# Optimization experiments

Measured on AMD Instinct MI355X. Metric: run time of the kernel, lower is better.

## Reference

```python
import jax, jax.numpy as jnp
import numpy as np

N_GRAPHS = 2048
BN_EPS = 1e-5


def _lin_init(k, fan_in, fan_out):
    kw, kb = jax.random.split(k)
    s = 1.0 / np.sqrt(fan_in)
    w = jax.random.uniform(kw, (fan_in, fan_out), minval=-s, maxval=s, dtype=jnp.float32)
    b = jax.random.uniform(kb, (fan_out,), minval=-s, maxval=s, dtype=jnp.float32)
    return w, b


def setup_inputs() -> dict:
    key = jax.random.key(0)
    ks = jax.random.split(key, 16)
    N, E, F, H, C = 100000, 600000, 7, 128, 2
    inp = {}
    inp["x"] = jax.random.normal(ks[0], (N, F), dtype=jnp.float32)
    inp["edge_index"] = jax.random.randint(ks[1], (2, E), 0, N)
    inp["edge_attr"] = jax.random.normal(ks[2], (E,), dtype=jnp.float32)  # ignored by GINConv
    inp["batch"] = jnp.sort(jax.random.randint(ks[3], (N,), 0, N_GRAPHS))
    # GINConv inner MLPs: [in, H, H]
    inp["g1_w1"], inp["g1_b1"] = _lin_init(ks[4], F, H)
    inp["g1_w2"], inp["g1_b2"] = _lin_init(ks[5], H, H)
    inp["g2_w1"], inp["g2_b1"] = _lin_init(ks[6], H, H)
    inp["g2_w2"], inp["g2_b2"] = _lin_init(ks[7], H, H)
    inp["g3_w1"], inp["g3_b1"] = _lin_init(ks[8], H, H)
    inp["g3_w2"], inp["g3_b2"] = _lin_init(ks[9], H, H)
    # JumpingKnowledge('cat') projection: 3H -> H
    inp["jk_w"], inp["jk_b"] = _lin_init(ks[10], 3 * H, H)
    # classifier MLP [H, H, C] with batch_norm on hidden layer
    inp["c1_w"], inp["c1_b"] = _lin_init(ks[11], H, H)
    inp["bn_g"] = jnp.ones((H,), jnp.float32)
    inp["bn_b"] = jnp.zeros((H,), jnp.float32)
    inp["c2_w"], inp["c2_b"] = _lin_init(ks[12], H, C)
    return inp


def reference(x, edge_index, edge_attr, batch,
              g1_w1, g1_b1, g1_w2, g1_b2,
              g2_w1, g2_b1, g2_w2, g2_b2,
              g3_w1, g3_b1, g3_w2, g3_b2,
              jk_w, jk_b, c1_w, c1_b, bn_g, bn_b, c2_w, c2_b):
    src, dst = edge_index[0], edge_index[1]
    N = x.shape[0]

    def gin_conv(h, w1, b1, w2, b2):
        # sum aggregation of neighbor messages; eps=0 -> (1+eps)*x + aggr = x + aggr
        agg = jax.ops.segment_sum(h[src], dst, num_segments=N)
        z = h + agg
        return jax.nn.relu(z @ w1 + b1) @ w2 + b2  # inner MLP, plain last layer

    # BasicGNN applies act (ReLU) after each conv; dropout=eval (identity)
    h1 = jax.nn.relu(gin_conv(x, g1_w1, g1_b1, g1_w2, g1_b2))
    h2 = jax.nn.relu(gin_conv(h1, g2_w1, g2_b1, g2_w2, g2_b2))
    h3 = jax.nn.relu(gin_conv(h2, g3_w1, g3_b1, g3_w2, g3_b2))

    h = jnp.concatenate([h1, h2, h3], axis=-1) @ jk_w + jk_b  # jk='cat' + final lin
    g = jax.ops.segment_sum(h, batch, num_segments=N_GRAPHS)  # global_add_pool -> [G, H]

    z = g @ c1_w + c1_b
    mu = z.mean(axis=0)
    var = z.var(axis=0)
    z = (z - mu) * jax.lax.rsqrt(var + BN_EPS) * bn_g + bn_b  # batch_norm (batch stats)
    z = jax.nn.relu(z)
    return z @ c2_w + c2_b  # [G, num_classes]
```

## Files before the change

kernel.cpp:

```cpp
#include <hip/hip_runtime.h>

#define NGRAPH 2048
#define EIDX_CAP 1024

typedef __attribute__((ext_vector_type(4))) float f32x4;
typedef __attribute__((ext_vector_type(8))) _Float16 h16x8;
typedef __attribute__((ext_vector_type(2))) _Float16 h16x2;

__global__ __launch_bounds__(256) void scan_onepass(
    const int* __restrict__ deg, int* __restrict__ rowstart, int* __restrict__ cursor,
    unsigned* __restrict__ scanst, int N, int E, int nchunk)
{
  __shared__ int tmp[256];
  __shared__ int sh_chunk;
  __shared__ int sh_exc;
  int tid = threadIdx.x;
  if (tid == 0) sh_chunk = (int)atomicAdd(&scanst[nchunk], 1u);
  __syncthreads();
  int cb = sh_chunk;
  int i = cb * 256 + tid;
  int v = (i < N) ? deg[i] : 0;
  tmp[tid] = v;
  __syncthreads();
#pragma unroll
  for (int off = 1; off < 256; off <<= 1) {
    int t = (tid >= off) ? tmp[tid - off] : 0;
    __syncthreads();
    tmp[tid] += t;
    __syncthreads();
  }
  int aggregate = tmp[255];

  if (tid == 0) {
    const unsigned VMASK = (1u << 30) - 1u;
    if (cb == 0) {
      atomicExch(&scanst[0], (2u << 30) | (unsigned)aggregate);
      sh_exc = 0;
    } else {
      atomicExch(&scanst[cb], (1u << 30) | (unsigned)aggregate);
      int excv = 0;
      int j = cb - 1;
      while (j >= 0) {
        unsigned s;
        do { s = atomicAdd(&scanst[j], 0u); } while ((s >> 30) == 0u);
        excv += (int)(s & VMASK);
        if ((s >> 30) == 2u) break;
        --j;
      }
      sh_exc = excv;
      atomicExch(&scanst[cb], (2u << 30) | (unsigned)(excv + aggregate));
    }
  }
  __syncthreads();
  int exc = sh_exc;
  if (i < N) {
    int rs = exc + tmp[tid] - v;
    rowstart[i] = rs;
    cursor[i] = rs;
  }
  if (cb == nchunk - 1 && tid == 0) rowstart[N] = E;
}

__global__ __launch_bounds__(256) void fill_eidx(
    const int* __restrict__ src, const int* __restrict__ dst,
    int* __restrict__ cursor, int* __restrict__ eidx, int E)
{
  int e = blockIdx.x * 256 + threadIdx.x;
  if (e >= E) return;
  int d = dst[e];
  int pos = atomicAdd(&cursor[d], 1);
  eidx[pos] = src[e];
}

struct WPs {
  const float* w[5];
  _Float16* hi[5];
  _Float16* lo[5];
};
__global__ __launch_bounds__(256) void prep_hist(
    WPs p, const float* __restrict__ x, _Float16* __restrict__ x8h, int N,
    const int* __restrict__ dst, int* __restrict__ deg, int E,
    const int* __restrict__ batch, int* __restrict__ gstart,
    float* __restrict__ bnstat)
{
  int g = blockIdx.x * 256 + threadIdx.x;
  if (g < E) {
    atomicAdd(&deg[dst[g]], 1);
    return;
  }
  int q = g - E;
  if (q < 5 * 16384) {
    int m = q >> 14;
    int j = q & 16383;
    int c = j >> 3, e = j & 7;
    int t = c >> 8, kc = (c >> 6) & 3, lane = c & 63;
    int n = t * 16 + (lane & 15);
    int k = kc * 32 + (lane >> 4) * 8 + e;
    float w = p.w[m][k * 128 + n];
    _Float16 h = (_Float16)w;
    p.hi[m][j] = h;
    p.lo[m][j] = (_Float16)(w - (float)h);
    return;
  }
  q -= 5 * 16384;
  if (q < N * 8) {
    int v = q >> 3, j = q & 7;
    x8h[q] = (_Float16)((j < 7) ? x[(long)v * 7 + j] : 0.f);
    return;
  }
  q -= N * 8;
  if (q < 256) { bnstat[q] = 0.f; return; }
  q -= 256;
  if (q < N) {
    int b = batch[q];
    int bp = (q > 0) ? batch[q - 1] : -1;
    for (int gg = bp + 1; gg <= b; ++gg) gstart[gg] = q;
    if (q == N - 1)
      for (int gg = b + 1; gg <= NGRAPH; ++gg) gstart[gg] = N;
  }
}

__device__ inline void mfma_pass(
    const _Float16* __restrict__ zbuf,
    const _Float16* __restrict__ Whi, const _Float16* __restrict__ Wlo,
    int rw, int m16, int quad, int lane, f32x4 acc[8])
{
  int r = rw + m16;
  const _Float16* zrow = &zbuf[r * 128];
#pragma unroll
  for (int kc = 0; kc < 4; ++kc) {
    int cidx = kc * 4 + quad;
    h16x8 ah = *(const h16x8*)&zrow[((cidx + r) & 15) * 8];
#pragma unroll
    for (int t = 0; t < 8; ++t) {
      long cb = ((t * 4 + kc) * 64 + lane) * 8;
      h16x8 bh = *(const h16x8*)&Whi[cb];
      h16x8 bl = *(const h16x8*)&Wlo[cb];
      acc[t] = __builtin_amdgcn_mfma_f32_16x16x32_f16(ah, bh, acc[t], 0, 0, 0);
      acc[t] = __builtin_amdgcn_mfma_f32_16x16x32_f16(ah, bl, acc[t], 0, 0, 0);
    }
  }
}

__global__ __launch_bounds__(256, 5) void fused_gin(
    const _Float16* __restrict__ H, const int* __restrict__ rowstart,
    const int* __restrict__ eidx,
    const _Float16* __restrict__ W1hi, const _Float16* __restrict__ W1lo,
    const float* __restrict__ B1,
    const _Float16* __restrict__ W2hi, const _Float16* __restrict__ W2lo,
    const float* __restrict__ B2,
    _Float16* __restrict__ Out, int M)
{
  __shared__ _Float16 zbuf[64 * 128];
  __shared__ int sh_rs[65];
  __shared__ int sh_ei[EIDX_CAP];
  int tid = threadIdx.x;
  int rbase = blockIdx.x * 64;

  if (tid < 65) {
    int v = rbase + tid;
    sh_rs[tid] = rowstart[(v < M) ? v : M];
  }
  __syncthreads();
  int e_begin = sh_rs[0];
  int cnt = sh_rs[64] - e_begin;
  if (cnt <= EIDX_CAP) {
    for (int i = tid; i < cnt; i += 256) sh_ei[i] = eidx[e_begin + i];
  }
  __syncthreads();

  {
    int sub = tid & 15;
    int ng = tid >> 4;
    const _Float16* Hc = H + sub * 8;
    if (cnt <= EIDX_CAP) {
#pragma unroll 1
      for (int it = 0; it < 4; ++it) {
        int r = it * 16 + ng;
        int v = rbase + r;
        int vc = (v < M) ? v : (M - 1);
        h16x8 sv = *(const h16x8*)&Hc[(long)vc * 128];
        float a0[8], a1[8];
#pragma unroll
        for (int j = 0; j < 8; ++j) { a0[j] = (float)sv[j]; a1[j] = 0.f; }
        int e = sh_rs[r] - e_begin;
        int e1 = sh_rs[r + 1] - e_begin;
#pragma unroll 1
        for (; e < e1; e += 8) {
          int last = e1 - 1;
          int s0 = sh_ei[e];
          int s1 = sh_ei[(e + 1 < e1) ? e + 1 : last];
          int s2 = sh_ei[(e + 2 < e1) ? e + 2 : last];
          int s3 = sh_ei[(e + 3 < e1) ? e + 3 : last];
          int s4 = sh_ei[(e + 4 < e1) ? e + 4 : last];
          int s5 = sh_ei[(e + 5 < e1) ? e + 5 : last];
          int s6 = sh_ei[(e + 6 < e1) ? e + 6 : last];
          int s7 = sh_ei[(e + 7 < e1) ? e + 7 : last];
          float m1 = (e + 1 < e1) ? 1.f : 0.f;
          float m2 = (e + 2 < e1) ? 1.f : 0.f;
          float m3 = (e + 3 < e1) ? 1.f : 0.f;
          float m4 = (e + 4 < e1) ? 1.f : 0.f;
          float m5 = (e + 5 < e1) ? 1.f : 0.f;
          float m6 = (e + 6 < e1) ? 1.f : 0.f;
          float m7 = (e + 7 < e1) ? 1.f : 0.f;
          h16x8 h0 = *(const h16x8*)&Hc[(long)s0 * 128];
          h16x8 h1 = *(const h16x8*)&Hc[(long)s1 * 128];
          h16x8 h2 = *(const h16x8*)&Hc[(long)s2 * 128];
          h16x8 h3 = *(const h16x8*)&Hc[(long)s3 * 128];
          h16x8 h4 = *(const h16x8*)&Hc[(long)s4 * 128];
          h16x8 h5 = *(const h16x8*)&Hc[(long)s5 * 128];
          h16x8 h6 = *(const h16x8*)&Hc[(long)s6 * 128];
          h16x8 h7 = *(const h16x8*)&Hc[(long)s7 * 128];
#pragma unroll
          for (int j = 0; j < 8; ++j) {
            a0[j] += (float)h0[j] + m2 * (float)h2[j] + m4 * (float)h4[j] + m6 * (float)h6[j];
            a1[j] += m1 * (float)h1[j] + m3 * (float)h3[j] + m5 * (float)h5[j] + m7 * (float)h7[j];
          }
        }
        h16x8 zo;
#pragma unroll
        for (int j = 0; j < 8; ++j) zo[j] = (_Float16)(a0[j] + a1[j]);
        *(h16x8*)&zbuf[r * 128 + ((sub + r) & 15) * 8] = zo;
      }
    } else {
#pragma unroll 1
      for (int it = 0; it < 4; ++it) {
        int r = it * 16 + ng;
        int v = rbase + r;
        int vc = (v < M) ? v : (M - 1);
        h16x8 sv = *(const h16x8*)&Hc[(long)vc * 128];
        float a0[8], a1[8];
#pragma unroll
        for (int j = 0; j < 8; ++j) { a0[j] = (float)sv[j]; a1[j] = 0.f; }
        int e = sh_rs[r], e1 = sh_rs[r + 1];
        for (; e + 2 <= e1; e += 2) {
          int s0 = eidx[e], s1 = eidx[e + 1];
          h16x8 h0 = *(const h16x8*)&Hc[(long)s0 * 128];
          h16x8 h1 = *(const h16x8*)&Hc[(long)s1 * 128];
#pragma unroll
          for (int j = 0; j < 8; ++j) { a0[j] += (float)h0[j]; a1[j] += (float)h1[j]; }
        }
        if (e < e1) {
          int s = eidx[e];
          h16x8 h = *(const h16x8*)&Hc[(long)s * 128];
#pragma unroll
          for (int j = 0; j < 8; ++j) a1[j] += (float)h[j];
        }
        h16x8 zo;
#pragma unroll
        for (int j = 0; j < 8; ++j) zo[j] = (_Float16)(a0[j] + a1[j]);
        *(h16x8*)&zbuf[r * 128 + ((sub + r) & 15) * 8] = zo;
      }
    }
  }
  __syncthreads();

  int lane = tid & 63;
  int wv = tid >> 6;
  int m16 = lane & 15;
  int quad = lane >> 4;
  int rw = wv * 16;

  f32x4 acc[8];
#pragma unroll
  for (int t = 0; t < 8; ++t) acc[t] = (f32x4){0.f, 0.f, 0.f, 0.f};
  mfma_pass(zbuf, W1hi, W1lo, rw, m16, quad, lane, acc);

  float bias[8];
#pragma unroll
  for (int t = 0; t < 8; ++t) bias[t] = B1[t * 16 + m16];

#pragma unroll
  for (int i = 0; i < 4; ++i) {
    int r = rw + quad * 4 + i;
#pragma unroll
    for (int t = 0; t < 8; ++t) {
      int col = t * 16 + m16;
      int cidx = col >> 3;
      zbuf[r * 128 + ((cidx + r) & 15) * 8 + (col & 7)] =
          (_Float16)fmaxf(acc[t][i] + bias[t], 0.f);
    }
  }

#pragma unroll
  for (int t = 0; t < 8; ++t) acc[t] = (f32x4){0.f, 0.f, 0.f, 0.f};
  mfma_pass(zbuf, W2hi, W2lo, rw, m16, quad, lane, acc);

#pragma unroll
  for (int t = 0; t < 8; ++t) bias[t] = B2[t * 16 + m16];

#pragma unroll
  for (int i = 0; i < 4; ++i) {
    int r = rw + quad * 4 + i;
#pragma unroll
    for (int t = 0; t < 8; ++t) {
      int col = t * 16 + m16;
      int cidx = col >> 3;
      zbuf[r * 128 + ((cidx + r) & 15) * 8 + (col & 7)] =
          (_Float16)fmaxf(acc[t][i] + bias[t], 0.f);
    }
  }
  {
    int rr2 = tid >> 2, c4 = tid & 3;
    int r = rbase + rr2;
    if (r < M) {
#pragma unroll
      for (int it = 0; it < 4; ++it) {
        int cidx = it * 4 + c4;
        h16x8 vv = *(const h16x8*)&zbuf[rr2 * 128 + ((cidx + rr2) & 15) * 8];
        *(h16x8*)&Out[(long)r * 128 + cidx * 8] = vv;
      }
    }
  }
}

__global__ __launch_bounds__(256, 8) void fused_l1(
    const _Float16* __restrict__ x8h, const int* __restrict__ rowstart,
    const int* __restrict__ eidx,
    const float* __restrict__ W1, const float* __restrict__ B1,
    const _Float16* __restrict__ W2hi, const _Float16* __restrict__ W2lo,
    const float* __restrict__ B2, _Float16* __restrict__ Out, int M)
{
  __shared__ _Float16 ybuf[64 * 128];
  __shared__ float z1s[64][8];
  int tid = threadIdx.x;
  int rbase = blockIdx.x * 64;

  {
    int node = tid >> 2, sub = tid & 3;
    int v = rbase + node;
    int vc = (v < M) ? v : (M - 1);
    float a[8];
    if (sub == 0) {
      h16x8 sv = *(const h16x8*)&x8h[(long)vc * 8];
#pragma unroll
      for (int j = 0; j < 8; ++j) a[j] = (float)sv[j];
    } else {
#pragma unroll
      for (int j = 0; j < 8; ++j) a[j] = 0.f;
    }
    int e0 = rowstart[vc], e1 = rowstart[vc + 1];
    int e = e0 + sub;
    for (; e + 4 < e1; e += 8) {
      int s0 = eidx[e], s1 = eidx[e + 4];
      h16x8 h0 = *(const h16x8*)&x8h[(long)s0 * 8];
      h16x8 h1 = *(const h16x8*)&x8h[(long)s1 * 8];
#pragma unroll
      for (int j = 0; j < 8; ++j) a[j] += (float)h0[j] + (float)h1[j];
    }
    if (e < e1) {
      int s = eidx[e];
      h16x8 h = *(const h16x8*)&x8h[(long)s * 8];
#pragma unroll
      for (int j = 0; j < 8; ++j) a[j] += (float)h[j];
    }
#pragma unroll
    for (int j = 0; j < 8; ++j) {
      a[j] += __shfl_xor(a[j], 1, 64);
      a[j] += __shfl_xor(a[j], 2, 64);
    }
    if (sub == 0) {
#pragma unroll
      for (int j = 0; j < 8; ++j) z1s[node][j] = a[j];
    }
  }
  __syncthreads();

  {
    int c = tid & 127;
    int cidx = c >> 3, celt = c & 7;
    int rh0 = (tid >> 7) * 32;
    float w1r[7];
#pragma unroll
    for (int k = 0; k < 7; ++k) w1r[k] = W1[k * 128 + c];
    float b1 = B1[c];
#pragma unroll 4
    for (int rr = 0; rr < 32; ++rr) {
      int r = rh0 + rr;
      const float* zp = z1s[r];
      float a = b1;
#pragma unroll
      for (int k = 0; k < 7; ++k) a += zp[k] * w1r[k];
      ybuf[r * 128 + ((cidx + r) & 15) * 8 + celt] = (_Float16)fmaxf(a, 0.f);
    }
  }
  __syncthreads();

  int lane = tid & 63;
  int wv = tid >> 6;
  int m16 = lane & 15;
  int quad = lane >> 4;
  int rw = wv * 16;

  f32x4 acc[8];
#pragma unroll
  for (int t = 0; t < 8; ++t) acc[t] = (f32x4){0.f, 0.f, 0.f, 0.f};
  mfma_pass(ybuf, W2hi, W2lo, rw, m16, quad, lane, acc);

  float bias[8];
#pragma unroll
  for (int t = 0; t < 8; ++t) bias[t] = B2[t * 16 + m16];

#pragma unroll
  for (int i = 0; i < 4; ++i) {
    int r = rw + quad * 4 + i;
#pragma unroll
    for (int t = 0; t < 8; ++t) {
      int col = t * 16 + m16;
      int cidx = col >> 3;
      ybuf[r * 128 + ((cidx + r) & 15) * 8 + (col & 7)] =
          (_Float16)fmaxf(acc[t][i] + bias[t], 0.f);
    }
  }
  {
    int rr2 = tid >> 2, c4 = tid & 3;
    int r = rbase + rr2;
    if (r < M) {
#pragma unroll
      for (int it = 0; it < 4; ++it) {
        int cidx = it * 4 + c4;
        h16x8 vv = *(const h16x8*)&ybuf[rr2 * 128 + ((cidx + rr2) & 15) * 8];
        *(h16x8*)&Out[(long)r * 128 + cidx * 8] = vv;
      }
    }
  }
}

__global__ __launch_bounds__(256) void pool_direct(
    const _Float16* __restrict__ H1, const _Float16* __restrict__ H2,
    const _Float16* __restrict__ H3, const int* __restrict__ gstart,
    float* __restrict__ P)
{
  __shared__ float red[3 * 16 * 8 * 4];
  int g = blockIdx.x;
  int s = gstart[g], e = gstart[g + 1];
  int tid = threadIdx.x;
  int wv = tid >> 6, lane = tid & 63;
  int tbl = lane >> 4;
  int ch = lane & 15;
  float a[8];
#pragma unroll
  for (int j = 0; j < 8; ++j) a[j] = 0.f;
  if (tbl < 3) {
    const _Float16* A = (tbl == 0) ? H1 : ((tbl == 1) ? H2 : H3);
    const _Float16* Ac = A + ch * 8;
    for (int r = s + wv; r < e; r += 4) {
      h16x8 v = *(const h16x8*)&Ac[(long)r * 128];
#pragma unroll
      for (int j = 0; j < 8; ++j) a[j] += (float)v[j];
    }
#pragma unroll
    for (int j = 0; j < 8; ++j) red[((tbl * 16 + ch) * 8 + j) * 4 + wv] = a[j];
  }
  __syncthreads();
  for (int t = tid; t < 384; t += 256) {
    float4 rv = *(const float4*)&red[t * 4];
    P[(long)g * 384 + t] = rv.x + rv.y + rv.z + rv.w;
  }
}

__global__ __launch_bounds__(256) void jk_gemm(
    const float* __restrict__ P, const int* __restrict__ gstart,
    const float* __restrict__ W, const float* __restrict__ B,
    float* __restrict__ G)
{
  __shared__ float pl[768];
  int tid = threadIdx.x, blk = blockIdx.x;
  for (int o = tid; o < 768; o += 256) pl[o] = P[(long)blk * 768 + o];
  __syncthreads();
  int rr = tid >> 7;
  int col = tid & 127;
  int row = blk * 2 + rr;
  float cntv = (float)(gstart[row + 1] - gstart[row]);
  float acc = cntv * B[col];
#pragma unroll 8
  for (int k = 0; k < 384; ++k)
    acc += pl[rr * 384 + k] * W[k * 128 + col];
  G[(long)row * 128 + col] = acc;
}

__global__ __launch_bounds__(256) void gemm_bn(
    const float* __restrict__ Z,
    const float* __restrict__ W, const float* __restrict__ B,
    float* __restrict__ Out, float* __restrict__ bnstat, int M)
{
  __shared__ float wlds[128 * 128];
  int tid = threadIdx.x;
  {
    const float4* Ws = (const float4*)W;
    float4* Wd = (float4*)wlds;
#pragma unroll
    for (int i = 0; i < 16; ++i) Wd[i * 256 + tid] = Ws[i * 256 + tid];
  }
  __syncthreads();

  int rg = tid >> 5;
  int c0 = (tid & 31) * 4;
  int rbase = blockIdx.x * 64 + rg * 8;

  float acc[8][4];
#pragma unroll
  for (int i = 0; i < 8; ++i)
#pragma unroll
    for (int j = 0; j < 4; ++j) acc[i][j] = 0.f;

#pragma unroll 2
  for (int kc = 0; kc < 128; kc += 4) {
    float zv[8][4];
#pragma unroll
    for (int i = 0; i < 8; ++i) {
      float4 z = *(const float4*)&Z[(long)(rbase + i) * 128 + kc];
      zv[i][0] = z.x; zv[i][1] = z.y; zv[i][2] = z.z; zv[i][3] = z.w;
    }
#pragma unroll
    for (int kk = 0; kk < 4; ++kk) {
      float4 w = *(const float4*)&wlds[(kc + kk) * 128 + c0];
#pragma unroll
      for (int i = 0; i < 8; ++i) {
        float z = zv[i][kk];
        acc[i][0] += z * w.x; acc[i][1] += z * w.y;
        acc[i][2] += z * w.z; acc[i][3] += z * w.w;
      }
    }
  }

  float4 b = *(const float4*)&B[c0];
  float s[4] = {0.f, 0.f, 0.f, 0.f};
  float s2[4] = {0.f, 0.f, 0.f, 0.f};
#pragma unroll
  for (int i = 0; i < 8; ++i) {
    float4 o;
    o.x = acc[i][0] + b.x; o.y = acc[i][1] + b.y;
    o.z = acc[i][2] + b.z; o.w = acc[i][3] + b.w;
    *(float4*)&Out[(long)(rbase + i) * 128 + c0] = o;
    s[0] += o.x; s[1] += o.y; s[2] += o.z; s[3] += o.w;
    s2[0] += o.x * o.x; s2[1] += o.y * o.y; s2[2] += o.z * o.z; s2[3] += o.w * o.w;
  }
#pragma unroll
  for (int j = 0; j < 4; ++j) {
    atomicAdd(&bnstat[c0 + j], s[j]);
    atomicAdd(&bnstat[128 + c0 + j], s2[j]);
  }
}

__global__ __launch_bounds__(256) void bn_final(
    const float* __restrict__ ZC, const float* __restrict__ bnstat,
    const float* __restrict__ gma, const float* __restrict__ bta,
    const float* __restrict__ W2, const float* __restrict__ B2, float* __restrict__ out)
{
  __shared__ float scl[128], shf[128];
  int tid = threadIdx.x;
  if (tid < 128) {
    float mu = bnstat[tid] * (1.f / NGRAPH);
    float var = bnstat[128 + tid] * (1.f / NGRAPH) - mu * mu;
    float rs = rsqrtf(var + 1e-5f);
    float sc = gma[tid] * rs;
    scl[tid] = sc;
    shf[tid] = bta[tid] - mu * sc;
  }
  __syncthreads();
  int g = blockIdx.x * 256 + tid;
  if (g >= NGRAPH) return;
  float a0 = B2[0], a1 = B2[1];
#pragma unroll 4
  for (int h = 0; h < 128; ++h) {
    float zn = ZC[(long)g * 128 + h] * scl[h] + shf[h];
    zn = fmaxf(zn, 0.f);
    a0 += zn * W2[2 * h];
    a1 += zn * W2[2 * h + 1];
  }
  out[2 * g] = a0;
  out[2 * g + 1] = a1;
}

extern "C" void kernel_launch(void* const* d_in, const int* in_sizes, int n_in,
                              void* d_out, int out_size, void* d_ws, size_t ws_size,
                              hipStream_t stream)
{
  const float* x    = (const float*)d_in[0];
  const int*   ei   = (const int*)d_in[1];
  const int*   batch = (const int*)d_in[3];
  const float* g1w1 = (const float*)d_in[4];  const float* g1b1 = (const float*)d_in[5];
  const float* g1w2 = (const float*)d_in[6];  const float* g1b2 = (const float*)d_in[7];
  const float* g2w1 = (const float*)d_in[8];  const float* g2b1 = (const float*)d_in[9];
  const float* g2w2 = (const float*)d_in[10]; const float* g2b2 = (const float*)d_in[11];
  const float* g3w1 = (const float*)d_in[12]; const float* g3b1 = (const float*)d_in[13];
  const float* g3w2 = (const float*)d_in[14]; const float* g3b2 = (const float*)d_in[15];
  const float* jkw  = (const float*)d_in[16]; const float* jkb  = (const float*)d_in[17];
  const float* c1w  = (const float*)d_in[18]; const float* c1b  = (const float*)d_in[19];
  const float* bng  = (const float*)d_in[20]; const float* bnb  = (const float*)d_in[21];
  const float* c2w  = (const float*)d_in[22]; const float* c2b  = (const float*)d_in[23];

  const int N = in_sizes[3];
  const int E = in_sizes[1] / 2;
  const int* src = ei;
  const int* dst = ei + E;

  char* w = (char*)d_ws;
  auto alloc = [&](size_t bytes) {
    char* p = w;
    w += (bytes + 255) & ~(size_t)255;
    return p;
  };
  _Float16* hA = (_Float16*)alloc((size_t)N * 128 * 2);
  _Float16* hB = (_Float16*)alloc((size_t)N * 128 * 2);
  _Float16* hC = (_Float16*)alloc((size_t)N * 128 * 2);
  _Float16* x8h = (_Float16*)alloc((size_t)N * 8 * 2);
  float* P       = (float*)alloc((size_t)NGRAPH * 384 * 4);
  float* bnstat  = (float*)alloc(256 * 4);
  float* gbuf = (float*)alloc((size_t)NGRAPH * 128 * 4);
  float* zc   = (float*)alloc((size_t)NGRAPH * 128 * 4);
  int* deg      = (int*)alloc((size_t)N * 4);
  unsigned* scanst = (unsigned*)alloc((size_t)1024 * 4);
  int* cursor   = (int*)alloc((size_t)N * 4);
  int* rowstart = (int*)alloc((size_t)(N + 1) * 4);
  int* eidx     = (int*)alloc((size_t)E * 4);
  int* gstart   = (int*)alloc((size_t)(NGRAPH + 1) * 4);
  _Float16* wtbuf = (_Float16*)alloc((size_t)5 * 2 * 16384 * 2);

  _Float16* WThi[5];
  _Float16* WTlo[5];
  for (int m = 0; m < 5; ++m) {
    WThi[m] = wtbuf + (size_t)m * 2 * 16384;
    WTlo[m] = WThi[m] + 16384;
  }

  const int nchunk = (N + 255) / 256;
  const int eb = (E + 255) / 256;

  hipMemsetAsync(deg, 0, (size_t)((char*)(scanst + 1024) - (char*)deg), stream);

  {
    WPs p;
    p.w[0] = g1w2; p.w[1] = g2w1; p.w[2] = g2w2; p.w[3] = g3w1; p.w[4] = g3w2;
    for (int m = 0; m < 5; ++m) { p.hi[m] = WThi[m]; p.lo[m] = WTlo[m]; }
    int total = E + 5 * 16384 + N * 8 + 256 + N;
    prep_hist<<<(total + 255) / 256, 256, 0, stream>>>(p, x, x8h, N, dst, deg, E,
                                                       batch, gstart, bnstat);
  }

  scan_onepass<<<nchunk, 256, 0, stream>>>(deg, rowstart, cursor, scanst, N, E, nchunk);
  fill_eidx<<<eb, 256, 0, stream>>>(src, dst, cursor, eidx, E);

  const int fBlocks = (N + 63) / 64;

  fused_l1<<<fBlocks, 256, 0, stream>>>(x8h, rowstart, eidx, g1w1, g1b1,
      WThi[0], WTlo[0], g1b2, hC, N);
  fused_gin<<<fBlocks, 256, 0, stream>>>(hC, rowstart, eidx,
      WThi[1], WTlo[1], g2b1, WThi[2], WTlo[2], g2b2, hB, N);
  fused_gin<<<fBlocks, 256, 0, stream>>>(hB, rowstart, eidx,
      WThi[3], WTlo[3], g3b1, WThi[4], WTlo[4], g3b2, hA, N);

  pool_direct<<<NGRAPH, 256, 0, stream>>>(hC, hB, hA, gstart, P);

  jk_gemm<<<NGRAPH / 2, 256, 0, stream>>>(P, gstart, jkw, jkb, gbuf);
  gemm_bn<<<NGRAPH / 64, 256, 0, stream>>>(gbuf, c1w, c1b, zc, bnstat, NGRAPH);
  bn_final<<<(NGRAPH + 255) / 256, 256, 0, stream>>>(zc, bnstat, bng, bnb, c2w, c2b, (float*)d_out);
}
```

Measured before the change: 410.9 us.

## Fuse global add pooling into GIN layer epilogues via atomics; retile tail kernels

Removes the separate pool_direct kernel. Each fused GIN/L1 block now sums its 64 output rows per graph segment out of LDS and atomically adds the partial sums into the pooled buffer P, which is zeroed by the existing memset. This avoids re-reading all three N×128 activation tensors from global memory, at the cost of global float atomics and an extra barrier in each layer. gemm_bn is also halved to 32 rows per block, and bn_final is restructured to stage rows in LDS with 4 threads per graph and a shuffle reduction, both to get more blocks in flight.

```diff
diff --git a/kernel.cpp b/kernel.cpp
--- a/kernel.cpp
+++ b/kernel.cpp
@@ -142,17 +142,41 @@
   }
 }
 
+__device__ inline void pool_epilogue(
+    const _Float16* buf, const int* sh_b, float* __restrict__ Pcol,
+    int tid, int rbase, int M)
+{
+  int c = tid & 127;
+  int cidx = c >> 3, celt = c & 7;
+  int i0 = (tid >> 7) * 32;
+  if (rbase + i0 >= M) return;
+  int iend = i0 + 32;
+  if (rbase + iend > M) iend = M - rbase;
+  float ps = 0.f;
+  int gcur = sh_b[i0];
+  for (int i = i0; i < iend; ++i) {
+    int gb = sh_b[i];
+    if (gb != gcur) {
+      atomicAdd(&Pcol[(long)gcur * 384 + c], ps);
+      ps = 0.f; gcur = gb;
+    }
+    ps += (float)buf[i * 128 + ((cidx + i) & 15) * 8 + celt];
+  }
+  atomicAdd(&Pcol[(long)gcur * 384 + c], ps);
+}
+
 __global__ __launch_bounds__(256, 5) void fused_gin(
     const _Float16* __restrict__ H, const int* __restrict__ rowstart,
-    const int* __restrict__ eidx,
+    const int* __restrict__ eidx, const int* __restrict__ batch,
     const _Float16* __restrict__ W1hi, const _Float16* __restrict__ W1lo,
     const float* __restrict__ B1,
     const _Float16* __restrict__ W2hi, const _Float16* __restrict__ W2lo,
     const float* __restrict__ B2,
-    _Float16* __restrict__ Out, int M)
+    _Float16* __restrict__ Out, float* __restrict__ Pcol, int M)
 {
   __shared__ _Float16 zbuf[64 * 128];
   __shared__ int sh_rs[65];
+  __shared__ int sh_b[64];
   __shared__ int sh_ei[EIDX_CAP];
   int tid = threadIdx.x;
   int rbase = blockIdx.x * 64;
@@ -160,6 +184,10 @@
   if (tid < 65) {
     int v = rbase + tid;
     sh_rs[tid] = rowstart[(v < M) ? v : M];
+  }
+  if (tid >= 128 && tid < 192) {
+    int v = rbase + tid - 128;
+    sh_b[tid - 128] = batch[(v < M) ? v : (M - 1)];
   }
   __syncthreads();
   int e_begin = sh_rs[0];
@@ -312,19 +340,29 @@
       }
     }
   }
+
+  __syncthreads();
+  pool_epilogue(zbuf, sh_b, Pcol, tid, rbase, M);
 }
 
 __global__ __launch_bounds__(256, 8) void fused_l1(
     const _Float16* __restrict__ x8h, const int* __restrict__ rowstart,
-    const int* __restrict__ eidx,
+    const int* __restrict__ eidx, const int* __restrict__ batch,
     const float* __restrict__ W1, const float* __restrict__ B1,
     const _Float16* __restrict__ W2hi, const _Float16* __restrict__ W2lo,
-    const float* __restrict__ B2, _Float16* __restrict__ Out, int M)
+    const float* __restrict__ B2, _Float16* __restrict__ Out,
+    float* __restrict__ Pcol, int M)
 {
   __shared__ _Float16 ybuf[64 * 128];
   __shared__ float z1s[64][8];
+  __shared__ int sh_b[64];
   int tid = threadIdx.x;
   int rbase = blockIdx.x * 64;
+
+  if (tid < 64) {
+    int v = rbase + tid;
+    sh_b[tid] = batch[(v < M) ? v : (M - 1)];
+  }
 
   {
     int node = tid >> 2, sub = tid & 3;
@@ -424,39 +462,9 @@
       }
     }
   }
-}
-
-__global__ __launch_bounds__(256) void pool_direct(
-    const _Float16* __restrict__ H1, const _Float16* __restrict__ H2,
-    const _Float16* __restrict__ H3, const int* __restrict__ gstart,
-    float* __restrict__ P)
-{
-  __shared__ float red[3 * 16 * 8 * 4];
-  int g = blockIdx.x;
-  int s = gstart[g], e = gstart[g + 1];
-  int tid = threadIdx.x;
-  int wv = tid >> 6, lane = tid & 63;
-  int tbl = lane >> 4;
-  int ch = lane & 15;
-  float a[8];
-#pragma unroll
-  for (int j = 0; j < 8; ++j) a[j] = 0.f;
-  if (tbl < 3) {
-    const _Float16* A = (tbl == 0) ? H1 : ((tbl == 1) ? H2 : H3);
-    const _Float16* Ac = A + ch * 8;
-    for (int r = s + wv; r < e; r += 4) {
-      h16x8 v = *(const h16x8*)&Ac[(long)r * 128];
-#pragma unroll
-      for (int j = 0; j < 8; ++j) a[j] += (float)v[j];
-    }
-#pragma unroll
-    for (int j = 0; j < 8; ++j) red[((tbl * 16 + ch) * 8 + j) * 4 + wv] = a[j];
-  }
-  __syncthreads();
-  for (int t = tid; t < 384; t += 256) {
-    float4 rv = *(const float4*)&red[t * 4];
-    P[(long)g * 384 + t] = rv.x + rv.y + rv.z + rv.w;
-  }
+
+  __syncthreads();
+  pool_epilogue(ybuf, sh_b, Pcol, tid, rbase, M);
 }
 
 __global__ __launch_bounds__(256) void jk_gemm(
@@ -496,19 +504,19 @@
 
   int rg = tid >> 5;
   int c0 = (tid & 31) * 4;
-  int rbase = blockIdx.x * 64 + rg * 8;
-
-  float acc[8][4];
-#pragma unroll
-  for (int i = 0; i < 8; ++i)
+  int rbase = blockIdx.x * 32 + rg * 4;
+
+  float acc[4][4];
+#pragma unroll
+  for (int i = 0; i < 4; ++i)
 #pragma unroll
     for (int j = 0; j < 4; ++j) acc[i][j] = 0.f;
 
 #pragma unroll 2
   for (int kc = 0; kc < 128; kc += 4) {
-    float zv[8][4];
-#pragma unroll
-    for (int i = 0; i < 8; ++i) {
+    float zv[4][4];
+#pragma unroll
+    for (int i = 0; i < 4; ++i) {
       float4 z = *(const float4*)&Z[(long)(rbase + i) * 128 + kc];
       zv[i][0] = z.x; zv[i][1] = z.y; zv[i][2] = z.z; zv[i][3] = z.w;
     }
@@ -516,7 +524,7 @@
     for (int kk = 0; kk < 4; ++kk) {
       float4 w = *(const float4*)&wlds[(kc + kk) * 128 + c0];
 #pragma unroll
-      for (int i = 0; i < 8; ++i) {
+      for (int i = 0; i < 4; ++i) {
         float z = zv[i][kk];
         acc[i][0] += z * w.x; acc[i][1] += z * w.y;
         acc[i][2] += z * w.z; acc[i][3] += z * w.w;
@@ -528,7 +536,7 @@
   float s[4] = {0.f, 0.f, 0.f, 0.f};
   float s2[4] = {0.f, 0.f, 0.f, 0.f};
 #pragma unroll
-  for (int i = 0; i < 8; ++i) {
+  for (int i = 0; i < 4; ++i) {
     float4 o;
     o.x = acc[i][0] + b.x; o.y = acc[i][1] + b.y;
     o.z = acc[i][2] + b.z; o.w = acc[i][3] + b.w;
@@ -549,6 +557,7 @@
     const float* __restrict__ W2, const float* __restrict__ B2, float* __restrict__ out)
 {
   __shared__ float scl[128], shf[128];
+  __shared__ float zl[64 * 132];
   int tid = threadIdx.x;
   if (tid < 128) {
     float mu = bnstat[tid] * (1.f / NGRAPH);
@@ -558,19 +567,29 @@
     scl[tid] = sc;
     shf[tid] = bta[tid] - mu * sc;
   }
-  __syncthreads();
-  int g = blockIdx.x * 256 + tid;
-  if (g >= NGRAPH) return;
-  float a0 = B2[0], a1 = B2[1];
-#pragma unroll 4
-  for (int h = 0; h < 128; ++h) {
-    float zn = ZC[(long)g * 128 + h] * scl[h] + shf[h];
+  int g0 = blockIdx.x * 64;
+  for (int i = tid; i < 64 * 128; i += 256) {
+    int r = i >> 7, c = i & 127;
+    zl[r * 132 + c] = ZC[(long)(g0 + r) * 128 + c];
+  }
+  __syncthreads();
+  int q = tid >> 2, sub = tid & 3;
+  int g = g0 + q;
+  float a0 = 0.f, a1 = 0.f;
+#pragma unroll 8
+  for (int hh = 0; hh < 32; ++hh) {
+    int h = sub + hh * 4;
+    float zn = zl[q * 132 + h] * scl[h] + shf[h];
     zn = fmaxf(zn, 0.f);
     a0 += zn * W2[2 * h];
     a1 += zn * W2[2 * h + 1];
   }
-  out[2 * g] = a0;
-  out[2 * g + 1] = a1;
+  a0 += __shfl_xor(a0, 1, 64); a0 += __shfl_xor(a0, 2, 64);
+  a1 += __shfl_xor(a1, 1, 64); a1 += __shfl_xor(a1, 2, 64);
+  if (sub == 0) {
+    out[2 * g] = a0 + B2[0];
+    out[2 * g + 1] = a1 + B2[1];
+  }
 }
 
 extern "C" void kernel_launch(void* const* d_in, const int* in_sizes, int n_in,
@@ -606,10 +625,10 @@
   _Float16* hB = (_Float16*)alloc((size_t)N * 128 * 2);
   _Float16* hC = (_Float16*)alloc((size_t)N * 128 * 2);
   _Float16* x8h = (_Float16*)alloc((size_t)N * 8 * 2);
-  float* P       = (float*)alloc((size_t)NGRAPH * 384 * 4);
   float* bnstat  = (float*)alloc(256 * 4);
   float* gbuf = (float*)alloc((size_t)NGRAPH * 128 * 4);
   float* zc   = (float*)alloc((size_t)NGRAPH * 128 * 4);
+  float* P       = (float*)alloc((size_t)NGRAPH * 384 * 4);
   int* deg      = (int*)alloc((size_t)N * 4);
   unsigned* scanst = (unsigned*)alloc((size_t)1024 * 4);
   int* cursor   = (int*)alloc((size_t)N * 4);
@@ -628,7 +647,7 @@
   const int nchunk = (N + 255) / 256;
   const int eb = (E + 255) / 256;
 
-  hipMemsetAsync(deg, 0, (size_t)((char*)(scanst + 1024) - (char*)deg), stream);
+  hipMemsetAsync(P, 0, (size_t)((char*)(scanst + 1024) - (char*)P), stream);
 
   {
     WPs p;
@@ -644,16 +663,14 @@
 
   const int fBlocks = (N + 63) / 64;
 
-  fused_l1<<<fBlocks, 256, 0, stream>>>(x8h, rowstart, eidx, g1w1, g1b1,
-      WThi[0], WTlo[0], g1b2, hC, N);
-  fused_gin<<<fBlocks, 256, 0, stream>>>(hC, rowstart, eidx,
-      WThi[1], WTlo[1], g2b1, WThi[2], WTlo[2], g2b2, hB, N);
-  fused_gin<<<fBlocks, 256, 0, stream>>>(hB, rowstart, eidx,
-      WThi[3], WTlo[3], g3b1, WThi[4], WTlo[4], g3b2, hA, N);
-
-  pool_direct<<<NGRAPH, 256, 0, stream>>>(hC, hB, hA, gstart, P);
+  fused_l1<<<fBlocks, 256, 0, stream>>>(x8h, rowstart, eidx, batch, g1w1, g1b1,
+      WThi[0], WTlo[0], g1b2, hC, P, N);
+  fused_gin<<<fBlocks, 256, 0, stream>>>(hC, rowstart, eidx, batch,
+      WThi[1], WTlo[1], g2b1, WThi[2], WTlo[2], g2b2, hB, P + 128, N);
+  fused_gin<<<fBlocks, 256, 0, stream>>>(hB, rowstart, eidx, batch,
+      WThi[3], WTlo[3], g3b1, WThi[4], WTlo[4], g3b2, hA, P + 256, N);
 
   jk_gemm<<<NGRAPH / 2, 256, 0, stream>>>(P, gstart, jkw, jkb, gbuf);
-  gemm_bn<<<NGRAPH / 64, 256, 0, stream>>>(gbuf, c1w, c1b, zc, bnstat, NGRAPH);
-  bn_final<<<(NGRAPH + 255) / 256, 256, 0, stream>>>(zc, bnstat, bng, bnb, c2w, c2b, (float*)d_out);
-}
+  gemm_bn<<<NGRAPH / 32, 256, 0, stream>>>(gbuf, c1w, c1b, zc, bnstat, NGRAPH);
+  bn_final<<<NGRAPH / 64, 256, 0, stream>>>(zc, bnstat, bng, bnb, c2w, c2b, (float*)d_out);
+}
```

Result: slower. 434.0 us (+5.6%).

## Fold JK projection and classifier linear into one precomputed weight

Applied to the files above, without the earlier changes.

Precomputes the product of the JK projection weight and the first classifier weight (and its bias) inside the prep kernel, so the pooled features go through a single 384x128 GEMM that also accumulates batch-norm statistics. This removes one kernel launch, the intermediate graph buffer, and a separate 128x128 GEMM. bn_final is restructured to stage rows in LDS and split each row across four lanes with shuffle reductions, giving more blocks. The change alters float summation order slightly and adds roughly 6M FMAs of weight-product work to the prep kernel.

```diff
diff --git a/kernel.cpp b/kernel.cpp
--- a/kernel.cpp
+++ b/kernel.cpp
@@ -81,7 +81,9 @@
     WPs p, const float* __restrict__ x, _Float16* __restrict__ x8h, int N,
     const int* __restrict__ dst, int* __restrict__ deg, int E,
     const int* __restrict__ batch, int* __restrict__ gstart,
-    float* __restrict__ bnstat)
+    float* __restrict__ bnstat,
+    const float* __restrict__ jkw, const float* __restrict__ jkb,
+    const float* __restrict__ c1w, float* __restrict__ wc, float* __restrict__ bcv)
 {
   int g = blockIdx.x * 256 + threadIdx.x;
   if (g < E) {
@@ -117,6 +119,25 @@
     for (int gg = bp + 1; gg <= b; ++gg) gstart[gg] = q;
     if (q == N - 1)
       for (int gg = b + 1; gg <= NGRAPH; ++gg) gstart[gg] = N;
+    return;
+  }
+  q -= N;
+  if (q < 384 * 128) {
+    int k = q >> 7, n = q & 127;
+    float acc = 0.f;
+#pragma unroll 8
+    for (int h = 0; h < 128; ++h)
+      acc += jkw[k * 128 + h] * c1w[h * 128 + n];
+    wc[q] = acc;
+    return;
+  }
+  q -= 384 * 128;
+  if (q < 128) {
+    float acc = 0.f;
+#pragma unroll 8
+    for (int h = 0; h < 128; ++h)
+      acc += jkb[h] * c1w[h * 128 + q];
+    bcv[q] = acc;
   }
 }
 
@@ -459,87 +480,47 @@
   }
 }
 
-__global__ __launch_bounds__(256) void jk_gemm(
+__global__ __launch_bounds__(256) void jk_bn(
     const float* __restrict__ P, const int* __restrict__ gstart,
-    const float* __restrict__ W, const float* __restrict__ B,
-    float* __restrict__ G)
-{
-  __shared__ float pl[768];
+    const float* __restrict__ Wc, const float* __restrict__ bc,
+    const float* __restrict__ c1b,
+    float* __restrict__ zc, float* __restrict__ bnstat)
+{
+  __shared__ float pl[8 * 384];
+  __shared__ float red[512];
   int tid = threadIdx.x, blk = blockIdx.x;
-  for (int o = tid; o < 768; o += 256) pl[o] = P[(long)blk * 768 + o];
-  __syncthreads();
-  int rr = tid >> 7;
-  int col = tid & 127;
-  int row = blk * 2 + rr;
-  float cntv = (float)(gstart[row + 1] - gstart[row]);
-  float acc = cntv * B[col];
-#pragma unroll 8
-  for (int k = 0; k < 384; ++k)
-    acc += pl[rr * 384 + k] * W[k * 128 + col];
-  G[(long)row * 128 + col] = acc;
-}
-
-__global__ __launch_bounds__(256) void gemm_bn(
-    const float* __restrict__ Z,
-    const float* __restrict__ W, const float* __restrict__ B,
-    float* __restrict__ Out, float* __restrict__ bnstat, int M)
-{
-  __shared__ float wlds[128 * 128];
-  int tid = threadIdx.x;
-  {
-    const float4* Ws = (const float4*)W;
-    float4* Wd = (float4*)wlds;
-#pragma unroll
-    for (int i = 0; i < 16; ++i) Wd[i * 256 + tid] = Ws[i * 256 + tid];
-  }
-  __syncthreads();
-
-  int rg = tid >> 5;
-  int c0 = (tid & 31) * 4;
-  int rbase = blockIdx.x * 64 + rg * 8;
-
-  float acc[8][4];
-#pragma unroll
-  for (int i = 0; i < 8; ++i)
-#pragma unroll
-    for (int j = 0; j < 4; ++j) acc[i][j] = 0.f;
-
-#pragma unroll 2
-  for (int kc = 0; kc < 128; kc += 4) {
-    float zv[8][4];
-#pragma unroll
-    for (int i = 0; i < 8; ++i) {
-      float4 z = *(const float4*)&Z[(long)(rbase + i) * 128 + kc];
-      zv[i][0] = z.x; zv[i][1] = z.y; zv[i][2] = z.z; zv[i][3] = z.w;
-    }
-#pragma unroll
-    for (int kk = 0; kk < 4; ++kk) {
-      float4 w = *(const float4*)&wlds[(kc + kk) * 128 + c0];
-#pragma unroll
-      for (int i = 0; i < 8; ++i) {
-        float z = zv[i][kk];
-        acc[i][0] += z * w.x; acc[i][1] += z * w.y;
-        acc[i][2] += z * w.z; acc[i][3] += z * w.w;
-      }
-    }
-  }
-
-  float4 b = *(const float4*)&B[c0];
-  float s[4] = {0.f, 0.f, 0.f, 0.f};
-  float s2[4] = {0.f, 0.f, 0.f, 0.f};
-#pragma unroll
-  for (int i = 0; i < 8; ++i) {
-    float4 o;
-    o.x = acc[i][0] + b.x; o.y = acc[i][1] + b.y;
-    o.z = acc[i][2] + b.z; o.w = acc[i][3] + b.w;
-    *(float4*)&Out[(long)(rbase + i) * 128 + c0] = o;
-    s[0] += o.x; s[1] += o.y; s[2] += o.z; s[3] += o.w;
-    s2[0] += o.x * o.x; s2[1] += o.y * o.y; s2[2] += o.z * o.z; s2[3] += o.w * o.w;
-  }
-#pragma unroll
-  for (int j = 0; j < 4; ++j) {
-    atomicAdd(&bnstat[c0 + j], s[j]);
-    atomicAdd(&bnstat[128 + c0 + j], s2[j]);
+  int r0 = blk * 8;
+  for (int o = tid; o < 8 * 384; o += 256)
+    pl[o] = P[(long)r0 * 384 + o];
+  __syncthreads();
+  int col = tid & 127, rg = tid >> 7;
+  float acc[4];
+  float b0 = bc[col], b1 = c1b[col];
+#pragma unroll
+  for (int i = 0; i < 4; ++i) {
+    int row = r0 + rg + 2 * i;
+    float cntv = (float)(gstart[row + 1] - gstart[row]);
+    acc[i] = cntv * b0 + b1;
+  }
+#pragma unroll 4
+  for (int k = 0; k < 384; ++k) {
+    float w = Wc[k * 128 + col];
+#pragma unroll
+    for (int i = 0; i < 4; ++i)
+      acc[i] += pl[(rg + 2 * i) * 384 + k] * w;
+  }
+  float s = 0.f, s2 = 0.f;
+#pragma unroll
+  for (int i = 0; i < 4; ++i) {
+    int row = r0 + rg + 2 * i;
+    zc[(long)row * 128 + col] = acc[i];
+    s += acc[i]; s2 += acc[i] * acc[i];
+  }
+  red[tid] = s; red[256 + tid] = s2;
+  __syncthreads();
+  if (tid < 128) {
+    atomicAdd(&bnstat[tid], red[tid] + red[tid + 128]);
+    atomicAdd(&bnstat[128 + tid], red[256 + tid] + red[256 + tid + 128]);
   }
 }
 
@@ -549,6 +530,7 @@
     const float* __restrict__ W2, const float* __restrict__ B2, float* __restrict__ out)
 {
   __shared__ float scl[128], shf[128];
+  __shared__ float zl[64 * 132];
   int tid = threadIdx.x;
   if (tid < 128) {
     float mu = bnstat[tid] * (1.f / NGRAPH);
@@ -558,19 +540,29 @@
     scl[tid] = sc;
     shf[tid] = bta[tid] - mu * sc;
   }
-  __syncthreads();
-  int g = blockIdx.x * 256 + tid;
-  if (g >= NGRAPH) return;
-  float a0 = B2[0], a1 = B2[1];
-#pragma unroll 4
-  for (int h = 0; h < 128; ++h) {
-    float zn = ZC[(long)g * 128 + h] * scl[h] + shf[h];
+  int g0 = blockIdx.x * 64;
+  for (int i = tid; i < 64 * 128; i += 256) {
+    int r = i >> 7, c = i & 127;
+    zl[r * 132 + c] = ZC[(long)(g0 + r) * 128 + c];
+  }
+  __syncthreads();
+  int q = tid >> 2, sub = tid & 3;
+  int g = g0 + q;
+  float a0 = 0.f, a1 = 0.f;
+#pragma unroll 8
+  for (int hh = 0; hh < 32; ++hh) {
+    int h = sub + hh * 4;
+    float zn = zl[q * 132 + h] * scl[h] + shf[h];
     zn = fmaxf(zn, 0.f);
     a0 += zn * W2[2 * h];
     a1 += zn * W2[2 * h + 1];
   }
-  out[2 * g] = a0;
-  out[2 * g + 1] = a1;
+  a0 += __shfl_xor(a0, 1, 64); a0 += __shfl_xor(a0, 2, 64);
+  a1 += __shfl_xor(a1, 1, 64); a1 += __shfl_xor(a1, 2, 64);
+  if (sub == 0) {
+    out[2 * g] = a0 + B2[0];
+    out[2 * g + 1] = a1 + B2[1];
+  }
 }
 
 extern "C" void kernel_launch(void* const* d_in, const int* in_sizes, int n_in,
@@ -608,8 +600,9 @@
   _Float16* x8h = (_Float16*)alloc((size_t)N * 8 * 2);
   float* P       = (float*)alloc((size_t)NGRAPH * 384 * 4);
   float* bnstat  = (float*)alloc(256 * 4);
-  float* gbuf = (float*)alloc((size_t)NGRAPH * 128 * 4);
   float* zc   = (float*)alloc((size_t)NGRAPH * 128 * 4);
+  float* wc   = (float*)alloc((size_t)384 * 128 * 4);
+  float* bcv  = (float*)alloc((size_t)128 * 4);
   int* deg      = (int*)alloc((size_t)N * 4);
   unsigned* scanst = (unsigned*)alloc((size_t)1024 * 4);
   int* cursor   = (int*)alloc((size_t)N * 4);
@@ -634,9 +627,10 @@
     WPs p;
     p.w[0] = g1w2; p.w[1] = g2w1; p.w[2] = g2w2; p.w[3] = g3w1; p.w[4] = g3w2;
     for (int m = 0; m < 5; ++m) { p.hi[m] = WThi[m]; p.lo[m] = WTlo[m]; }
-    int total = E + 5 * 16384 + N * 8 + 256 + N;
+    int total = E + 5 * 16384 + N * 8 + 256 + N + 384 * 128 + 128;
     prep_hist<<<(total + 255) / 256, 256, 0, stream>>>(p, x, x8h, N, dst, deg, E,
-                                                       batch, gstart, bnstat);
+                                                       batch, gstart, bnstat,
+                                                       jkw, jkb, c1w, wc, bcv);
   }
 
   scan_onepass<<<nchunk, 256, 0, stream>>>(deg, rowstart, cursor, scanst, N, E, nchunk);
@@ -653,7 +647,6 @@
 
   pool_direct<<<NGRAPH, 256, 0, stream>>>(hC, hB, hA, gstart, P);
 
-  jk_gemm<<<NGRAPH / 2, 256, 0, stream>>>(P, gstart, jkw, jkb, gbuf);
-  gemm_bn<<<NGRAPH / 64, 256, 0, stream>>>(gbuf, c1w, c1b, zc, bnstat, NGRAPH);
-  bn_final<<<(NGRAPH + 255) / 256, 256, 0, stream>>>(zc, bnstat, bng, bnb, c2w, c2b, (float*)d_out);
-}
+  jk_bn<<<NGRAPH / 8, 256, 0, stream>>>(P, gstart, wc, bcv, c1b, zc, bnstat);
+  bn_final<<<NGRAPH / 64, 256, 0, stream>>>(zc, bnstat, bng, bnb, c2w, c2b, (float*)d_out);
+}
```

New measurement: 395.2 us. -3.8%, faster.
